# Kernel tuning notes

Hardware: AMD Instinct MI355X
Metric: run time of the kernel (lower is better)

## Reference

```python
import jax, jax.numpy as jnp
import numpy as np

NUM_EXPERTS = 8
TOP_K = 2
RMS_EPS = 1e-6
SCALING = NUM_EXPERTS / TOP_K


def setup_inputs() -> dict:
    key = jax.random.key(0)
    ks = jax.random.split(key, 6)
    B, S, H, I, E = 4, 2048, 2048, 1024, NUM_EXPERTS
    return {
        "hidden_states": jax.random.normal(ks[0], (B, S, H), dtype=jnp.float32),
        "norm_w": jnp.ones((H,), dtype=jnp.float32),
        "router_w": jax.random.normal(ks[1], (E, H), dtype=jnp.float32) * 0.02,
        "gate_w": jax.random.normal(ks[2], (E, I, H), dtype=jnp.float32) * 0.02,
        "up_w": jax.random.normal(ks[3], (E, I, H), dtype=jnp.float32) * 0.02,
        "down_w": jax.random.normal(ks[4], (E, H, I), dtype=jnp.float32) * 0.02,
    }


def reference(hidden_states, norm_w, router_w, gate_w, up_w, down_w):
    B, S, H = hidden_states.shape
    T = B * S
    flat = hidden_states.reshape(T, H)

    # RMSNorm on router input (fp32 math, as in torch module)
    x32 = flat.astype(jnp.float32)
    var = jnp.mean(x32 * x32, axis=-1, keepdims=True)
    router_input = norm_w * (x32 * jax.lax.rsqrt(var + RMS_EPS))

    # Router: softmax -> top-k -> renormalize
    logits = router_input @ router_w.T                     # [T, E]
    probs = jax.nn.softmax(logits, axis=-1)
    topw, topi = jax.lax.top_k(probs, TOP_K)               # [T, K]
    topw = topw / jnp.sum(topw, axis=-1, keepdims=True)

    # Expert combine: per-token weight for expert e (0 if not selected).
    # Running every token through every expert with weight-0 masking is
    # mathematically identical to the gather/scatter dispatch.
    out = jnp.zeros_like(flat)
    for e in range(NUM_EXPERTS):
        w_e = jnp.sum(jnp.where(topi == e, topw, 0.0), axis=-1)   # [T]
        g = flat @ gate_w[e].T                                    # [T, I]
        u = flat @ up_w[e].T                                      # [T, I]
        o = (jax.nn.silu(g) * u) @ down_w[e].T                    # [T, H]
        out = out + o * w_e[:, None]

    student_output = out.reshape(B, S, H) * SCALING

    # Aux load-balancing loss (training path)
    importance = jnp.sum(probs, axis=0) / T                       # [E]
    load = jnp.sum(topi[..., None] == jnp.arange(NUM_EXPERTS), axis=(0, 1)) / (T * TOP_K)
    aux_loss = jnp.sum(importance * load.astype(jnp.float32)) * NUM_EXPERTS

    return student_output, aux_loss
```

## Files before the change

kernel.cpp:

```cpp
#include <hip/hip_runtime.h>
#include <hip/hip_bf16.h>
#include <cstdint>

#define T_TOKENS 8192
#define H_DIM 2048
#define I_DIM 1024
#define N_EXPERTS 8
#define PAIRS (T_TOKENS * 2)
#define TOT_TILES 144
#define TOT_ROWS (TOT_TILES * 128)

using f32x4 = __attribute__((ext_vector_type(4))) float;
using bfv   = __attribute__((ext_vector_type(8))) short;
using u16x8 = __attribute__((ext_vector_type(8))) unsigned short;

typedef __attribute__((address_space(3))) unsigned int lds_u32;
typedef __attribute__((address_space(1))) unsigned int glb_u32;

__device__ __forceinline__ void gll16(const void* g, void* l) {
  __builtin_amdgcn_global_load_lds((const glb_u32*)g, (lds_u32*)l, 16, 0, 0);
}
#define SB0() __builtin_amdgcn_sched_barrier(0)
#define BAR() __builtin_amdgcn_s_barrier()

__device__ inline unsigned short f2bf(float f) {
  unsigned int u = __float_as_uint(f);
  u += 0x7FFFu + ((u >> 16) & 1u);
  return (unsigned short)(u >> 16);
}

__global__ __launch_bounds__(256) void moe_convert_kernel(
    const float* __restrict__ src, unsigned short* __restrict__ dst, int n8) {
  int i = blockIdx.x * 256 + threadIdx.x;
  if (i >= n8) return;
  size_t o = (size_t)i * 8;
  f32x4 a = *reinterpret_cast<const f32x4*>(src + o);
  f32x4 b = *reinterpret_cast<const f32x4*>(src + o + 4);
  u16x8 r = {f2bf(a[0]), f2bf(a[1]), f2bf(a[2]), f2bf(a[3]),
             f2bf(b[0]), f2bf(b[1]), f2bf(b[2]), f2bf(b[3])};
  *reinterpret_cast<u16x8*>(dst + o) = r;
}

__global__ __launch_bounds__(256) void moe_router_kernel(
    const float* __restrict__ X, const float* __restrict__ norm_w,
    const float* __restrict__ rw, float* __restrict__ probs,
    float* __restrict__ topw, int* __restrict__ topi,
    unsigned int* __restrict__ counts, unsigned short* __restrict__ Xb) {
  int t = blockIdx.x;
  int tid = threadIdx.x;
  const float* x = X + (size_t)t * H_DIM;
  int base = tid * 8;
  f32x4 v0 = *reinterpret_cast<const f32x4*>(x + base);
  f32x4 v1 = *reinterpret_cast<const f32x4*>(x + base + 4);
  u16x8 bx = {f2bf(v0[0]), f2bf(v0[1]), f2bf(v0[2]), f2bf(v0[3]),
              f2bf(v1[0]), f2bf(v1[1]), f2bf(v1[2]), f2bf(v1[3])};
  *reinterpret_cast<u16x8*>(Xb + (size_t)t * H_DIM + base) = bx;
  f32x4 nw0 = *reinterpret_cast<const f32x4*>(norm_w + base);
  f32x4 nw1 = *reinterpret_cast<const f32x4*>(norm_w + base + 4);
  float vals[9];
  vals[0] = v0[0]*v0[0] + v0[1]*v0[1] + v0[2]*v0[2] + v0[3]*v0[3]
          + v1[0]*v1[0] + v1[1]*v1[1] + v1[2]*v1[2] + v1[3]*v1[3];
  f32x4 a0 = v0 * nw0, a1 = v1 * nw1;
#pragma unroll
  for (int e = 0; e < 8; ++e) {
    const float* r = rw + e * H_DIM + base;
    f32x4 r0 = *reinterpret_cast<const f32x4*>(r);
    f32x4 r1 = *reinterpret_cast<const f32x4*>(r + 4);
    f32x4 d = a0 * r0 + a1 * r1;
    vals[e + 1] = d[0] + d[1] + d[2] + d[3];
  }
#pragma unroll
  for (int v = 0; v < 9; ++v) {
    float s = vals[v];
#pragma unroll
    for (int off = 32; off > 0; off >>= 1) s += __shfl_xor(s, off);
    vals[v] = s;
  }
  __shared__ float red[4][9];
  int lane = tid & 63, w = tid >> 6;
  if (lane == 0) {
#pragma unroll
    for (int v = 0; v < 9; ++v) red[w][v] = vals[v];
  }
  __syncthreads();
  if (tid == 0) {
    float tot[9];
#pragma unroll
    for (int v = 0; v < 9; ++v) tot[v] = red[0][v] + red[1][v] + red[2][v] + red[3][v];
    float rs = rsqrtf(tot[0] / (float)H_DIM + 1e-6f);
    float lg[8], mx = -1e30f;
#pragma unroll
    for (int e = 0; e < 8; ++e) { lg[e] = tot[e + 1] * rs; mx = fmaxf(mx, lg[e]); }
    float pe[8], sum = 0.f;
#pragma unroll
    for (int e = 0; e < 8; ++e) { pe[e] = expf(lg[e] - mx); sum += pe[e]; }
    float inv = 1.f / sum;
#pragma unroll
    for (int e = 0; e < 8; ++e) { pe[e] *= inv; probs[t * 8 + e] = pe[e]; }
    int b1 = 0; float p1 = pe[0];
#pragma unroll
    for (int e = 1; e < 8; ++e) if (pe[e] > p1) { p1 = pe[e]; b1 = e; }
    int b2 = -1; float p2 = -1.f;
#pragma unroll
    for (int e = 0; e < 8; ++e) if (e != b1 && pe[e] > p2) { p2 = pe[e]; b2 = e; }
    float wsum = p1 + p2;
    topw[t * 2] = p1 / wsum;
    topw[t * 2 + 1] = p2 / wsum;
    topi[t * 2] = b1;
    topi[t * 2 + 1] = b2;
    atomicAdd(&counts[b1], 1u);
    atomicAdd(&counts[8 + b2], 1u);
  }
}

__global__ __launch_bounds__(256) void moe_importance_kernel(
    const float* __restrict__ probs, float* __restrict__ impSum) {
  int e = blockIdx.x, tid = threadIdx.x;
  float s = 0.f;
  for (int t = tid; t < T_TOKENS; t += 256) s += probs[t * 8 + e];
  __shared__ float red[256];
  red[tid] = s;
  __syncthreads();
  for (int st = 128; st > 0; st >>= 1) {
    if (tid < st) red[tid] += red[tid + st];
    __syncthreads();
  }
  if (tid == 0) impSum[e] = red[0];
}

__global__ void moe_offsets_aux_kernel(const unsigned int* __restrict__ counts,
                                       const float* __restrict__ impSum,
                                       int* __restrict__ tileOff,
                                       float* __restrict__ out_aux) {
  if (threadIdx.x == 0 && blockIdx.x == 0) {
    int acc = 0;
    for (int b = 0; b < 16; ++b) {
      tileOff[b] = acc;
      acc += (int)((counts[b] + 127u) >> 7);
    }
    tileOff[16] = acc;
    float a = 0.f;
    for (int e = 0; e < 8; ++e) {
      float load = (float)(counts[e] + counts[8 + e]) / (float)PAIRS;
      a += (impSum[e] / (float)T_TOKENS) * load;
    }
    out_aux[0] = a * (float)N_EXPERTS;
  }
}

__global__ __launch_bounds__(256) void moe_assign_kernel(
    const int* __restrict__ topi, const int* __restrict__ tileOff,
    unsigned int* __restrict__ cursors, int* __restrict__ row2pair) {
  int p = blockIdx.x * 256 + threadIdx.x;
  if (p >= PAIRS) return;
  int b = topi[p] + 8 * (p & 1);
  unsigned int pos = atomicAdd(&cursors[b], 1u);
  row2pair[tileOff[b] * 128 + (int)pos] = p;
}


__global__ __launch_bounds__(256, 2) void moe_stage_a(
    const unsigned short* __restrict__ Xb,
    const unsigned short* __restrict__ Wg, const unsigned short* __restrict__ Wu,
    const int* __restrict__ row2pair, const int* __restrict__ tileOff,
    unsigned int* __restrict__ workCtr, unsigned short* __restrict__ P) {
  __shared__ __align__(16) unsigned short sAB[2][12288];
  __shared__ int sTok[128];
  __shared__ int sWork;
  const int tid = threadIdx.x;
  const int lane = tid & 63, w = tid >> 6;
  const int lrow = lane & 15, grp = lane >> 4;
  const int s8 = ((tid & 3) ^ ((tid >> 2) & 3)) << 3;
  const int rsw = (grp ^ (lane & 3)) << 3;
  const int nTiles = tileOff[16];
  const int nWork = nTiles * 8;

  for (;;) {
    if (tid == 0) sWork = (int)atomicAdd(workCtr, 1u);
    __syncthreads();
    const int item = sWork;
    if (item >= nWork) break;
    const int mt = item % nTiles;
    const int nt = item / nTiles;
    int b = 0;
#pragma unroll
    for (int k = 1; k < 16; ++k) if (tileOff[k] <= mt) b = k;
    const int e = b & 7;
    const int row0 = mt * 128;
    if (tid < 128) {
      int pr = row2pair[row0 + tid];
      sTok[tid] = (pr >= 0) ? (pr >> 1) : 0;
    }
    __syncthreads();

    const size_t wbase = (size_t)e * ((size_t)I_DIM * H_DIM);
    const unsigned short* src[6];
#pragma unroll
    for (int it = 0; it < 2; ++it) {
      int ra = it * 64 + (tid >> 2);
      src[it] = Xb + (size_t)sTok[ra] * H_DIM + s8;
    }
#pragma unroll
    for (int it = 2; it < 6; ++it) {
      int c = (it - 2) * 64 + (tid >> 2);
      int wq = c >> 6, r6 = c & 63;
      int irow = nt * 128 + wq * 32 + (r6 & 31);
      const unsigned short* basep = (r6 >> 5) ? Wu : Wg;
      src[it] = basep + wbase + (size_t)irow * H_DIM + s8;
    }

    f32x4 acc[8][4] = {};

#pragma unroll
    for (int i = 0; i < 6; ++i)
      gll16(src[i], (void*)&sAB[0][(i * 256 + tid) * 8]);

    int cur = 0;
#pragma unroll 1
    for (int kk = 0; kk < 64; ++kk) {
      if (kk < 63) {
#pragma unroll
        for (int i = 0; i < 6; ++i)
          gll16(src[i] + ((kk + 1) << 5), (void*)&sAB[cur ^ 1][(i * 256 + tid) * 8]);
        SB0();
        asm volatile("s_waitcnt vmcnt(6)" ::: "memory");
      } else {
        asm volatile("s_waitcnt vmcnt(0)" ::: "memory");
      }
      SB0();
      BAR();
      SB0();
      bfv af[8], bf[4];
#pragma unroll
      for (int m = 0; m < 8; ++m)
        af[m] = *reinterpret_cast<const bfv*>(&sAB[cur][(m * 16 + lrow) * 32 + rsw]);
#pragma unroll
      for (int n = 0; n < 4; ++n)
        bf[n] = *reinterpret_cast<const bfv*>(&sAB[cur][4096 + (w * 64 + n * 16 + lrow) * 32 + rsw]);
      __builtin_amdgcn_s_setprio(1);
#pragma unroll
      for (int m = 0; m < 8; ++m)
#pragma unroll
        for (int n = 0; n < 4; ++n)
          acc[m][n] = __builtin_amdgcn_mfma_f32_16x16x32_bf16(af[m], bf[n], acc[m][n], 0, 0, 0);
      __builtin_amdgcn_s_setprio(0);
      SB0();
      BAR();
      cur ^= 1;
    }

#pragma unroll
    for (int m = 0; m < 8; ++m) {
#pragma unroll
      for (int n = 0; n < 2; ++n) {
#pragma unroll
        for (int j = 0; j < 4; ++j) {
          float g = acc[m][n][j];
          float uu = acc[m][n + 2][j];
          float pv = (g / (1.f + expf(-g))) * uu;
          int row = row0 + m * 16 + grp * 4 + j;
          int col = nt * 128 + w * 32 + n * 16 + lrow;
          P[(size_t)row * I_DIM + col] = f2bf(pv);
        }
      }
    }
  }
}

__global__ __launch_bounds__(256, 2) void moe_stage_b(
    const unsigned short* __restrict__ Pb, const unsigned short* __restrict__ Wd,
    const int* __restrict__ row2pair, const int* __restrict__ tileOff,
    const float* __restrict__ topw, unsigned int* __restrict__ workCtr,
    float* __restrict__ out, int phase) {
  __shared__ __align__(16) unsigned short sAB[2][12288];
  __shared__ int sPair[128];
  __shared__ int sWork;
  const int tid = threadIdx.x;
  const int lane = tid & 63, w = tid >> 6;
  const int lrow = lane & 15, grp = lane >> 4;
  const int s8 = ((tid & 3) ^ ((tid >> 2) & 3)) << 3;
  const int rsw = (grp ^ (lane & 3)) << 3;
  const int t0 = phase ? tileOff[8] : 0;
  const int t1 = phase ? tileOff[16] : tileOff[8];
  const int nTiles = t1 - t0;
  const int nWork = nTiles * 8;

  for (;;) {
    if (tid == 0) sWork = (int)atomicAdd(workCtr, 1u);
    __syncthreads();
    const int item = sWork;
    if (item >= nWork) break;
    const int mt = t0 + item % nTiles;
    const int nt = item / nTiles;
    int b = 0;
#pragma unroll
    for (int k = 1; k < 16; ++k) if (tileOff[k] <= mt) b = k;
    const int e = b & 7;
    const int row0 = mt * 128, h0 = nt * 256;
    if (tid < 128) sPair[tid] = row2pair[row0 + tid];
    __syncthreads();

    const unsigned short* src[6];
#pragma unroll
    for (int it = 0; it < 2; ++it) {
      int ra = it * 64 + (tid >> 2);
      src[it] = Pb + (size_t)(row0 + ra) * I_DIM + s8;
    }
#pragma unroll
    for (int it = 2; it < 6; ++it) {
      int c = (it - 2) * 64 + (tid >> 2);
      src[it] = Wd + (size_t)e * ((size_t)H_DIM * I_DIM) + (size_t)(h0 + c) * I_DIM + s8;
    }

    f32x4 acc[8][4] = {};

#pragma unroll
    for (int i = 0; i < 6; ++i)
      gll16(src[i], (void*)&sAB[0][(i * 256 + tid) * 8]);

    int cur = 0;
#pragma unroll 1
    for (int kk = 0; kk < 32; ++kk) {
      if (kk < 31) {
#pragma unroll
        for (int i = 0; i < 6; ++i)
          gll16(src[i] + ((kk + 1) << 5), (void*)&sAB[cur ^ 1][(i * 256 + tid) * 8]);
        SB0();
        asm volatile("s_waitcnt vmcnt(6)" ::: "memory");
      } else {
        asm volatile("s_waitcnt vmcnt(0)" ::: "memory");
      }
      SB0();
      BAR();
      SB0();
      bfv af[8], bf[4];
#pragma unroll
      for (int m = 0; m < 8; ++m)
        af[m] = *reinterpret_cast<const bfv*>(&sAB[cur][(m * 16 + lrow) * 32 + rsw]);
#pragma unroll
      for (int n = 0; n < 4; ++n)
        bf[n] = *reinterpret_cast<const bfv*>(&sAB[cur][4096 + (w * 64 + n * 16 + lrow) * 32 + rsw]);
      __builtin_amdgcn_s_setprio(1);
#pragma unroll
      for (int m = 0; m < 8; ++m)
#pragma unroll
        for (int n = 0; n < 4; ++n)
          acc[m][n] = __builtin_amdgcn_mfma_f32_16x16x32_bf16(af[m], bf[n], acc[m][n], 0, 0, 0);
      __builtin_amdgcn_s_setprio(0);
      SB0();
      BAR();
      cur ^= 1;
    }

#pragma unroll
    for (int m = 0; m < 8; ++m) {
#pragma unroll
      for (int j = 0; j < 4; ++j) {
        int rl = m * 16 + grp * 4 + j;
        int pr = sPair[rl];
        if (pr < 0) continue;
        float wgt = topw[pr] * 4.f;
        float* orow = out + (size_t)(pr >> 1) * H_DIM + h0 + w * 64 + lrow;
        if (phase) {
#pragma unroll
          for (int n = 0; n < 4; ++n) orow[n * 16] += wgt * acc[m][n][j];
        } else {
#pragma unroll
          for (int n = 0; n < 4; ++n) orow[n * 16] = wgt * acc[m][n][j];
        }
      }
    }
  }
}

extern "C" void kernel_launch(void* const* d_in, const int* in_sizes, int n_in,
                              void* d_out, int out_size, void* d_ws, size_t ws_size,
                              hipStream_t stream) {
  const float* X = (const float*)d_in[0];
  const float* norm_w = (const float*)d_in[1];
  const float* router_w = (const float*)d_in[2];
  const float* gate_w = (const float*)d_in[3];
  const float* up_w = (const float*)d_in[4];
  const float* down_w = (const float*)d_in[5];
  float* out = (float*)d_out;

  char* ws = (char*)d_ws;
  unsigned short* P = (unsigned short*)(ws);
  float* probs = (float*)(ws + 37748736);
  float* topw = (float*)(ws + 38010880);
  int* topi = (int*)(ws + 38076416);
  int* row2pair = (int*)(ws + 38141952);
  char* ctrl = ws + 38215680;
  unsigned int* counts = (unsigned int*)(ctrl);
  unsigned int* cursors = (unsigned int*)(ctrl + 64);
  float* impSum = (float*)(ctrl + 128);
  int* tileOff = (int*)(ctrl + 192);
  unsigned int* wcA = (unsigned int*)(ctrl + 384);
  unsigned int* wcB0 = (unsigned int*)(ctrl + 388);
  unsigned int* wcB1 = (unsigned int*)(ctrl + 392);
  unsigned short* W1 = (unsigned short*)(ws + 38216192);
  unsigned short* W2 = (unsigned short*)(ws + 71770624);
  unsigned short* Xb = (unsigned short*)(ws + 105325056);

  hipMemsetAsync(ctrl, 0, 512, stream);
  hipMemsetAsync(row2pair, 0xFF, (size_t)TOT_ROWS * 4, stream);

  const int N8 = (N_EXPERTS * I_DIM * H_DIM) / 8;
  moe_convert_kernel<<<N8 / 256, 256, 0, stream>>>(gate_w, W1, N8);
  moe_convert_kernel<<<N8 / 256, 256, 0, stream>>>(up_w, W2, N8);

  moe_router_kernel<<<T_TOKENS, 256, 0, stream>>>(X, norm_w, router_w, probs, topw, topi,
                                                  counts, Xb);
  moe_importance_kernel<<<N_EXPERTS, 256, 0, stream>>>(probs, impSum);
  moe_offsets_aux_kernel<<<1, 64, 0, stream>>>(counts, impSum, tileOff, out + 16777216);
  moe_assign_kernel<<<PAIRS / 256, 256, 0, stream>>>(topi, tileOff, cursors, row2pair);

  moe_stage_a<<<512, 256, 0, stream>>>(Xb, W1, W2, row2pair, tileOff, wcA, P);
  moe_convert_kernel<<<N8 / 256, 256, 0, stream>>>(down_w, W1, N8);
  moe_stage_b<<<512, 256, 0, stream>>>(P, W1, row2pair, tileOff, topw, wcB0, out, 0);
  moe_stage_b<<<512, 256, 0, stream>>>(P, W1, row2pair, tileOff, topw, wcB1, out, 1);
}
```

Before: 707.1 us.

## Store LDS tiles in MFMA fragment order and raise GEMM occupancy to three blocks

Both expert GEMM kernels now load global data straight into LDS in the order the MFMA operands need, so each lane reads one contiguous 16-byte fragment instead of going through the XOR-swizzled row layout. Separately, launch bounds go from 2 to 3 blocks per CU and the persistent grids grow from 512 to 768 blocks, to hide more latency. The new layout makes each lane's global load 16 bytes from a different row, which may coalesce worse. Fitting three blocks per CU also limits VGPRs and could cause spills, since each wave holds a 128-float accumulator.

```diff
diff --git a/kernel.cpp b/kernel.cpp
--- a/kernel.cpp
+++ b/kernel.cpp
@@ -159,7 +159,7 @@
 }
 
 
-__global__ __launch_bounds__(256, 2) void moe_stage_a(
+__global__ __launch_bounds__(256, 3) void moe_stage_a(
     const unsigned short* __restrict__ Xb,
     const unsigned short* __restrict__ Wg, const unsigned short* __restrict__ Wu,
     const int* __restrict__ row2pair, const int* __restrict__ tileOff,
@@ -170,8 +170,6 @@
   const int tid = threadIdx.x;
   const int lane = tid & 63, w = tid >> 6;
   const int lrow = lane & 15, grp = lane >> 4;
-  const int s8 = ((tid & 3) ^ ((tid >> 2) & 3)) << 3;
-  const int rsw = (grp ^ (lane & 3)) << 3;
   const int nTiles = tileOff[16];
   const int nWork = nTiles * 8;
 
@@ -196,17 +194,21 @@
     const size_t wbase = (size_t)e * ((size_t)I_DIM * H_DIM);
     const unsigned short* src[6];
 #pragma unroll
-    for (int it = 0; it < 2; ++it) {
-      int ra = it * 64 + (tid >> 2);
-      src[it] = Xb + (size_t)sTok[ra] * H_DIM + s8;
-    }
-#pragma unroll
-    for (int it = 2; it < 6; ++it) {
-      int c = (it - 2) * 64 + (tid >> 2);
-      int wq = c >> 6, r6 = c & 63;
+    for (int i = 0; i < 2; ++i) {
+      int idx = i * 256 + tid;
+      int l = idx & 63;
+      int row = (idx >> 6) * 16 + (l & 15);
+      src[i] = Xb + (size_t)sTok[row] * H_DIM + ((l >> 4) << 3);
+    }
+#pragma unroll
+    for (int i = 2; i < 6; ++i) {
+      int idx = (i - 2) * 256 + tid;
+      int l = idx & 63;
+      int brow = (idx >> 6) * 16 + (l & 15);
+      int wq = brow >> 6, r6 = brow & 63;
       int irow = nt * 128 + wq * 32 + (r6 & 31);
       const unsigned short* basep = (r6 >> 5) ? Wu : Wg;
-      src[it] = basep + wbase + (size_t)irow * H_DIM + s8;
+      src[i] = basep + wbase + (size_t)irow * H_DIM + ((l >> 4) << 3);
     }
 
     f32x4 acc[8][4] = {};
@@ -233,10 +235,10 @@
       bfv af[8], bf[4];
 #pragma unroll
       for (int m = 0; m < 8; ++m)
-        af[m] = *reinterpret_cast<const bfv*>(&sAB[cur][(m * 16 + lrow) * 32 + rsw]);
+        af[m] = *reinterpret_cast<const bfv*>(&sAB[cur][(m * 64 + lane) * 8]);
 #pragma unroll
       for (int n = 0; n < 4; ++n)
-        bf[n] = *reinterpret_cast<const bfv*>(&sAB[cur][4096 + (w * 64 + n * 16 + lrow) * 32 + rsw]);
+        bf[n] = *reinterpret_cast<const bfv*>(&sAB[cur][4096 + ((w * 4 + n) * 64 + lane) * 8]);
       __builtin_amdgcn_s_setprio(1);
 #pragma unroll
       for (int m = 0; m < 8; ++m)
@@ -267,7 +269,7 @@
   }
 }
 
-__global__ __launch_bounds__(256, 2) void moe_stage_b(
+__global__ __launch_bounds__(256, 3) void moe_stage_b(
     const unsigned short* __restrict__ Pb, const unsigned short* __restrict__ Wd,
     const int* __restrict__ row2pair, const int* __restrict__ tileOff,
     const float* __restrict__ topw, unsigned int* __restrict__ workCtr,
@@ -278,8 +280,6 @@
   const int tid = threadIdx.x;
   const int lane = tid & 63, w = tid >> 6;
   const int lrow = lane & 15, grp = lane >> 4;
-  const int s8 = ((tid & 3) ^ ((tid >> 2) & 3)) << 3;
-  const int rsw = (grp ^ (lane & 3)) << 3;
   const int t0 = phase ? tileOff[8] : 0;
   const int t1 = phase ? tileOff[16] : tileOff[8];
   const int nTiles = t1 - t0;
@@ -302,14 +302,19 @@
 
     const unsigned short* src[6];
 #pragma unroll
-    for (int it = 0; it < 2; ++it) {
-      int ra = it * 64 + (tid >> 2);
-      src[it] = Pb + (size_t)(row0 + ra) * I_DIM + s8;
-    }
-#pragma unroll
-    for (int it = 2; it < 6; ++it) {
-      int c = (it - 2) * 64 + (tid >> 2);
-      src[it] = Wd + (size_t)e * ((size_t)H_DIM * I_DIM) + (size_t)(h0 + c) * I_DIM + s8;
+    for (int i = 0; i < 2; ++i) {
+      int idx = i * 256 + tid;
+      int l = idx & 63;
+      int row = (idx >> 6) * 16 + (l & 15);
+      src[i] = Pb + (size_t)(row0 + row) * I_DIM + ((l >> 4) << 3);
+    }
+#pragma unroll
+    for (int i = 2; i < 6; ++i) {
+      int idx = (i - 2) * 256 + tid;
+      int l = idx & 63;
+      int brow = (idx >> 6) * 16 + (l & 15);
+      src[i] = Wd + (size_t)e * ((size_t)H_DIM * I_DIM) +
+               (size_t)(h0 + brow) * I_DIM + ((l >> 4) << 3);
     }
 
     f32x4 acc[8][4] = {};
@@ -336,10 +341,10 @@
       bfv af[8], bf[4];
 #pragma unroll
       for (int m = 0; m < 8; ++m)
-        af[m] = *reinterpret_cast<const bfv*>(&sAB[cur][(m * 16 + lrow) * 32 + rsw]);
+        af[m] = *reinterpret_cast<const bfv*>(&sAB[cur][(m * 64 + lane) * 8]);
 #pragma unroll
       for (int n = 0; n < 4; ++n)
-        bf[n] = *reinterpret_cast<const bfv*>(&sAB[cur][4096 + (w * 64 + n * 16 + lrow) * 32 + rsw]);
+        bf[n] = *reinterpret_cast<const bfv*>(&sAB[cur][4096 + ((w * 4 + n) * 64 + lane) * 8]);
       __builtin_amdgcn_s_setprio(1);
 #pragma unroll
       for (int m = 0; m < 8; ++m)
@@ -415,8 +420,8 @@
   moe_offsets_aux_kernel<<<1, 64, 0, stream>>>(counts, impSum, tileOff, out + 16777216);
   moe_assign_kernel<<<PAIRS / 256, 256, 0, stream>>>(topi, tileOff, cursors, row2pair);
 
-  moe_stage_a<<<512, 256, 0, stream>>>(Xb, W1, W2, row2pair, tileOff, wcA, P);
+  moe_stage_a<<<768, 256, 0, stream>>>(Xb, W1, W2, row2pair, tileOff, wcA, P);
   moe_convert_kernel<<<N8 / 256, 256, 0, stream>>>(down_w, W1, N8);
-  moe_stage_b<<<512, 256, 0, stream>>>(P, W1, row2pair, tileOff, topw, wcB0, out, 0);
-  moe_stage_b<<<512, 256, 0, stream>>>(P, W1, row2pair, tileOff, topw, wcB1, out, 1);
-}
+  moe_stage_b<<<768, 256, 0, stream>>>(P, W1, row2pair, tileOff, topw, wcB0, out, 0);
+  moe_stage_b<<<768, 256, 0, stream>>>(P, W1, row2pair, tileOff, topw, wcB1, out, 1);
+}
```

Result: slower. 1.412 ms (+99.7%).

## Shrink N tile to 128 and deepen K step to 64 in MoE GEMMs

Applied to the files above, without the earlier changes.

Both expert GEMM kernels change from a 128x256 output tile with a K step of 32 to a 128x128 tile with a K step of 64. The LDS layout and swizzle are rebuilt for 64-wide rows, and each K stage now issues two MFMA sub-steps. Work items per tile double, which gives more blocks for load balancing and halves the barrier count per tile. The cost is lower arithmetic intensity: the A tile is reloaded for twice as many N tiles, and the LDS footprint grows.

```diff
diff --git a/kernel.cpp b/kernel.cpp
--- a/kernel.cpp
+++ b/kernel.cpp
@@ -164,16 +164,17 @@
     const unsigned short* __restrict__ Wg, const unsigned short* __restrict__ Wu,
     const int* __restrict__ row2pair, const int* __restrict__ tileOff,
     unsigned int* __restrict__ workCtr, unsigned short* __restrict__ P) {
-  __shared__ __align__(16) unsigned short sAB[2][12288];
+  __shared__ __align__(16) unsigned short sAB[2][16384];
   __shared__ int sTok[128];
   __shared__ int sWork;
   const int tid = threadIdx.x;
   const int lane = tid & 63, w = tid >> 6;
   const int lrow = lane & 15, grp = lane >> 4;
-  const int s8 = ((tid & 3) ^ ((tid >> 2) & 3)) << 3;
-  const int rsw = (grp ^ (lane & 3)) << 3;
+  const int sub = lane >> 3;
+  const int kcs = ((lane & 7) ^ sub) << 3;
+  const int cx = (lane & 7) << 3;
   const int nTiles = tileOff[16];
-  const int nWork = nTiles * 8;
+  const int nWork = nTiles * 16;
 
   for (;;) {
     if (tid == 0) sWork = (int)atomicAdd(workCtr, 1u);
@@ -194,56 +195,61 @@
     __syncthreads();
 
     const size_t wbase = (size_t)e * ((size_t)I_DIM * H_DIM);
-    const unsigned short* src[6];
-#pragma unroll
-    for (int it = 0; it < 2; ++it) {
-      int ra = it * 64 + (tid >> 2);
-      src[it] = Xb + (size_t)sTok[ra] * H_DIM + s8;
-    }
-#pragma unroll
-    for (int it = 2; it < 6; ++it) {
-      int c = (it - 2) * 64 + (tid >> 2);
-      int wq = c >> 6, r6 = c & 63;
-      int irow = nt * 128 + wq * 32 + (r6 & 31);
-      const unsigned short* basep = (r6 >> 5) ? Wu : Wg;
-      src[it] = basep + wbase + (size_t)irow * H_DIM + s8;
-    }
-
-    f32x4 acc[8][4] = {};
-
-#pragma unroll
-    for (int i = 0; i < 6; ++i)
+    const unsigned short* src[8];
+#pragma unroll
+    for (int i = 0; i < 4; ++i) {
+      int row = i * 32 + 8 * w + sub;
+      src[i] = Xb + (size_t)sTok[row] * H_DIM + kcs;
+    }
+#pragma unroll
+    for (int i = 4; i < 8; ++i) {
+      int brow = (i - 4) * 32 + 8 * w + sub;
+      int wq = brow >> 5, r5 = brow & 31;
+      int ic = nt * 64 + wq * 16 + (r5 & 15);
+      const unsigned short* bp = (r5 & 16) ? Wu : Wg;
+      src[i] = bp + wbase + (size_t)ic * H_DIM + kcs;
+    }
+
+    f32x4 acc[8][2] = {};
+
+#pragma unroll
+    for (int i = 0; i < 8; ++i)
       gll16(src[i], (void*)&sAB[0][(i * 256 + tid) * 8]);
 
     int cur = 0;
 #pragma unroll 1
-    for (int kk = 0; kk < 64; ++kk) {
-      if (kk < 63) {
-#pragma unroll
-        for (int i = 0; i < 6; ++i)
-          gll16(src[i] + ((kk + 1) << 5), (void*)&sAB[cur ^ 1][(i * 256 + tid) * 8]);
+    for (int kk = 0; kk < 32; ++kk) {
+      if (kk < 31) {
+#pragma unroll
+        for (int i = 0; i < 8; ++i)
+          gll16(src[i] + ((kk + 1) << 6), (void*)&sAB[cur ^ 1][(i * 256 + tid) * 8]);
         SB0();
-        asm volatile("s_waitcnt vmcnt(6)" ::: "memory");
+        asm volatile("s_waitcnt vmcnt(8)" ::: "memory");
       } else {
         asm volatile("s_waitcnt vmcnt(0)" ::: "memory");
       }
       SB0();
       BAR();
       SB0();
-      bfv af[8], bf[4];
-#pragma unroll
-      for (int m = 0; m < 8; ++m)
-        af[m] = *reinterpret_cast<const bfv*>(&sAB[cur][(m * 16 + lrow) * 32 + rsw]);
-#pragma unroll
-      for (int n = 0; n < 4; ++n)
-        bf[n] = *reinterpret_cast<const bfv*>(&sAB[cur][4096 + (w * 64 + n * 16 + lrow) * 32 + rsw]);
-      __builtin_amdgcn_s_setprio(1);
-#pragma unroll
-      for (int m = 0; m < 8; ++m)
-#pragma unroll
-        for (int n = 0; n < 4; ++n)
-          acc[m][n] = __builtin_amdgcn_mfma_f32_16x16x32_bf16(af[m], bf[n], acc[m][n], 0, 0, 0);
-      __builtin_amdgcn_s_setprio(0);
+#pragma unroll
+      for (int ks = 0; ks < 2; ++ks) {
+        const int co = ((ks * 4 + grp) << 3) ^ cx;
+        bfv af[8], bf[2];
+#pragma unroll
+        for (int m = 0; m < 8; ++m)
+          af[m] = *reinterpret_cast<const bfv*>(&sAB[cur][(m * 16 + lrow) * 64 + co]);
+#pragma unroll
+        for (int n = 0; n < 2; ++n)
+          bf[n] = *reinterpret_cast<const bfv*>(
+              &sAB[cur][8192 + (w * 32 + n * 16 + lrow) * 64 + co]);
+        __builtin_amdgcn_s_setprio(1);
+#pragma unroll
+        for (int m = 0; m < 8; ++m)
+#pragma unroll
+          for (int n = 0; n < 2; ++n)
+            acc[m][n] = __builtin_amdgcn_mfma_f32_16x16x32_bf16(af[m], bf[n], acc[m][n], 0, 0, 0);
+        __builtin_amdgcn_s_setprio(0);
+      }
       SB0();
       BAR();
       cur ^= 1;
@@ -252,16 +258,13 @@
 #pragma unroll
     for (int m = 0; m < 8; ++m) {
 #pragma unroll
-      for (int n = 0; n < 2; ++n) {
-#pragma unroll
-        for (int j = 0; j < 4; ++j) {
-          float g = acc[m][n][j];
-          float uu = acc[m][n + 2][j];
-          float pv = (g / (1.f + expf(-g))) * uu;
-          int row = row0 + m * 16 + grp * 4 + j;
-          int col = nt * 128 + w * 32 + n * 16 + lrow;
-          P[(size_t)row * I_DIM + col] = f2bf(pv);
-        }
+      for (int j = 0; j < 4; ++j) {
+        float g = acc[m][0][j];
+        float uu = acc[m][1][j];
+        float pv = (g / (1.f + expf(-g))) * uu;
+        int row = row0 + m * 16 + grp * 4 + j;
+        int col = nt * 64 + w * 16 + lrow;
+        P[(size_t)row * I_DIM + col] = f2bf(pv);
       }
     }
   }
@@ -272,18 +275,19 @@
     const int* __restrict__ row2pair, const int* __restrict__ tileOff,
     const float* __restrict__ topw, unsigned int* __restrict__ workCtr,
     float* __restrict__ out, int phase) {
-  __shared__ __align__(16) unsigned short sAB[2][12288];
+  __shared__ __align__(16) unsigned short sAB[2][16384];
   __shared__ int sPair[128];
   __shared__ int sWork;
   const int tid = threadIdx.x;
   const int lane = tid & 63, w = tid >> 6;
   const int lrow = lane & 15, grp = lane >> 4;
-  const int s8 = ((tid & 3) ^ ((tid >> 2) & 3)) << 3;
-  const int rsw = (grp ^ (lane & 3)) << 3;
+  const int sub = lane >> 3;
+  const int kcs = ((lane & 7) ^ sub) << 3;
+  const int cx = (lane & 7) << 3;
   const int t0 = phase ? tileOff[8] : 0;
   const int t1 = phase ? tileOff[16] : tileOff[8];
   const int nTiles = t1 - t0;
-  const int nWork = nTiles * 8;
+  const int nWork = nTiles * 16;
 
   for (;;) {
     if (tid == 0) sWork = (int)atomicAdd(workCtr, 1u);
@@ -296,57 +300,62 @@
 #pragma unroll
     for (int k = 1; k < 16; ++k) if (tileOff[k] <= mt) b = k;
     const int e = b & 7;
-    const int row0 = mt * 128, h0 = nt * 256;
+    const int row0 = mt * 128, h0 = nt * 128;
     if (tid < 128) sPair[tid] = row2pair[row0 + tid];
     __syncthreads();
 
-    const unsigned short* src[6];
-#pragma unroll
-    for (int it = 0; it < 2; ++it) {
-      int ra = it * 64 + (tid >> 2);
-      src[it] = Pb + (size_t)(row0 + ra) * I_DIM + s8;
-    }
-#pragma unroll
-    for (int it = 2; it < 6; ++it) {
-      int c = (it - 2) * 64 + (tid >> 2);
-      src[it] = Wd + (size_t)e * ((size_t)H_DIM * I_DIM) + (size_t)(h0 + c) * I_DIM + s8;
-    }
-
-    f32x4 acc[8][4] = {};
-
-#pragma unroll
-    for (int i = 0; i < 6; ++i)
+    const unsigned short* src[8];
+#pragma unroll
+    for (int i = 0; i < 4; ++i) {
+      int row = i * 32 + 8 * w + sub;
+      src[i] = Pb + (size_t)(row0 + row) * I_DIM + kcs;
+    }
+#pragma unroll
+    for (int i = 4; i < 8; ++i) {
+      int brow = (i - 4) * 32 + 8 * w + sub;
+      src[i] = Wd + (size_t)e * ((size_t)H_DIM * I_DIM) + (size_t)(h0 + brow) * I_DIM + kcs;
+    }
+
+    f32x4 acc[8][2] = {};
+
+#pragma unroll
+    for (int i = 0; i < 8; ++i)
       gll16(src[i], (void*)&sAB[0][(i * 256 + tid) * 8]);
 
     int cur = 0;
 #pragma unroll 1
-    for (int kk = 0; kk < 32; ++kk) {
-      if (kk < 31) {
-#pragma unroll
-        for (int i = 0; i < 6; ++i)
-          gll16(src[i] + ((kk + 1) << 5), (void*)&sAB[cur ^ 1][(i * 256 + tid) * 8]);
+    for (int kk = 0; kk < 16; ++kk) {
+      if (kk < 15) {
+#pragma unroll
+        for (int i = 0; i < 8; ++i)
+          gll16(src[i] + ((kk + 1) << 6), (void*)&sAB[cur ^ 1][(i * 256 + tid) * 8]);
         SB0();
-        asm volatile("s_waitcnt vmcnt(6)" ::: "memory");
+        asm volatile("s_waitcnt vmcnt(8)" ::: "memory");
       } else {
         asm volatile("s_waitcnt vmcnt(0)" ::: "memory");
       }
       SB0();
       BAR();
       SB0();
-      bfv af[8], bf[4];
-#pragma unroll
-      for (int m = 0; m < 8; ++m)
-        af[m] = *reinterpret_cast<const bfv*>(&sAB[cur][(m * 16 + lrow) * 32 + rsw]);
-#pragma unroll
-      for (int n = 0; n < 4; ++n)
-        bf[n] = *reinterpret_cast<const bfv*>(&sAB[cur][4096 + (w * 64 + n * 16 + lrow) * 32 + rsw]);
-      __builtin_amdgcn_s_setprio(1);
-#pragma unroll
-      for (int m = 0; m < 8; ++m)
-#pragma unroll
-        for (int n = 0; n < 4; ++n)
-          acc[m][n] = __builtin_amdgcn_mfma_f32_16x16x32_bf16(af[m], bf[n], acc[m][n], 0, 0, 0);
-      __builtin_amdgcn_s_setprio(0);
+#pragma unroll
+      for (int ks = 0; ks < 2; ++ks) {
+        const int co = ((ks * 4 + grp) << 3) ^ cx;
+        bfv af[8], bf[2];
+#pragma unroll
+        for (int m = 0; m < 8; ++m)
+          af[m] = *reinterpret_cast<const bfv*>(&sAB[cur][(m * 16 + lrow) * 64 + co]);
+#pragma unroll
+        for (int n = 0; n < 2; ++n)
+          bf[n] = *reinterpret_cast<const bfv*>(
+              &sAB[cur][8192 + (w * 32 + n * 16 + lrow) * 64 + co]);
+        __builtin_amdgcn_s_setprio(1);
+#pragma unroll
+        for (int m = 0; m < 8; ++m)
+#pragma unroll
+          for (int n = 0; n < 2; ++n)
+            acc[m][n] = __builtin_amdgcn_mfma_f32_16x16x32_bf16(af[m], bf[n], acc[m][n], 0, 0, 0);
+        __builtin_amdgcn_s_setprio(0);
+      }
       SB0();
       BAR();
       cur ^= 1;
@@ -360,13 +369,13 @@
         int pr = sPair[rl];
         if (pr < 0) continue;
         float wgt = topw[pr] * 4.f;
-        float* orow = out + (size_t)(pr >> 1) * H_DIM + h0 + w * 64 + lrow;
+        float* orow = out + (size_t)(pr >> 1) * H_DIM + h0 + w * 32 + lrow;
         if (phase) {
 #pragma unroll
-          for (int n = 0; n < 4; ++n) orow[n * 16] += wgt * acc[m][n][j];
+          for (int n = 0; n < 2; ++n) orow[n * 16] += wgt * acc[m][n][j];
         } else {
 #pragma unroll
-          for (int n = 0; n < 4; ++n) orow[n * 16] = wgt * acc[m][n][j];
+          for (int n = 0; n < 2; ++n) orow[n * 16] = wgt * acc[m][n][j];
         }
       }
     }
```

After: 715.7 us. No clear change (+1.2%).
